# Kernel tuning notes

Measured on AMD Instinct MI355X. Metric: run time of the kernel, lower is better.

Reference implementation:

```python
import jax, jax.numpy as jnp
import numpy as np

LEAK = 0.2   # LeakyReLU slope in CVAE
T = 0.07     # MoCo temperature
TOPK = 2
DISK = 15


def _mlp2(x, Wa, ba, Wb, bb):
    # Linear -> ReLU -> Linear -> ReLU (MoCo encoders)
    return jax.nn.relu(jax.nn.relu(x @ Wa + ba) @ Wb + bb)


def setup_inputs() -> dict:
    key = jax.random.key(0)
    ks = jax.random.split(key, 32)
    B, R, V, F, L = 16384, 512, 1000, 300, 512

    def gn(k, shape, scale=0.05):
        return jax.random.normal(k, shape, dtype=jnp.float32) * scale

    inp = {}
    inp["logits"] = jax.random.normal(ks[0], (B, R), dtype=jnp.float32)
    inp["rels"] = jax.random.randint(ks[1], (R, 2), 0, V, dtype=jnp.int64)
    inp["rel_dict"] = jax.random.normal(ks[2], (V, F), dtype=jnp.float32)
    inp["eps1"] = jax.random.normal(ks[3], (B, L), dtype=jnp.float32)  # eps in ae.forward
    inp["eps2"] = jax.random.normal(ks[4], (B, L), dtype=jnp.float32)  # eps for z_
    # CVAE params (feature_size=300, class_size=300, latent_size=512)
    inp["W1"] = gn(ks[5], (F + F, 512)); inp["b1"] = jnp.zeros((512,), jnp.float32)
    inp["Wmu"] = gn(ks[6], (512, L));   inp["bmu"] = jnp.zeros((L,), jnp.float32)
    inp["Wls"] = gn(ks[7], (512, L));   inp["bls"] = jnp.zeros((L,), jnp.float32)
    inp["W3"] = gn(ks[8], (L + F, 512)); inp["b3"] = jnp.zeros((512,), jnp.float32)
    inp["W4"] = gn(ks[9], (512, F));    inp["b4"] = jnp.zeros((F,), jnp.float32)
    # MoCo encoder_inp (== encoder_k, since momentum update of identical params is a no-op)
    inp["iW1"] = gn(ks[10], (F, 512)); inp["ib1"] = jnp.zeros((512,), jnp.float32)
    inp["iW2"] = gn(ks[11], (512, 512)); inp["ib2"] = jnp.zeros((512,), jnp.float32)
    # MoCo encoder_z
    inp["zW1"] = gn(ks[12], (512, 512)); inp["zb1"] = jnp.zeros((512,), jnp.float32)
    inp["zW2"] = gn(ks[13], (512, 512)); inp["zb2"] = jnp.zeros((512,), jnp.float32)
    return inp


def reference(logits, rels, rel_dict, eps1, eps2,
              W1, b1, Wmu, bmu, Wls, bls, W3, b3, W4, b4,
              iW1, ib1, iW2, ib2, zW1, zb1, zW2, zb2):
    B = logits.shape[0]
    # sort descending / ascending over relation classes
    idx_desc = jnp.argsort(-logits, axis=1)
    idx_asc = jnp.argsort(logits, axis=1)
    top = idx_desc[:, :TOPK]        # [B,2]
    dis = idx_asc[:, :DISK]         # [B,15]

    keys = rels[:, 1]               # [R] indices into rel_dict
    # gathered features are all .detach()-ed in the original code
    pos1 = jax.lax.stop_gradient(rel_dict[keys[top[:, 0]]])   # [B,300]
    pos2 = jax.lax.stop_gradient(rel_dict[keys[top[:, 1]]])   # [B,300]
    neg = jax.lax.stop_gradient(rel_dict[keys[dis]])          # [B,15,300]

    # ---- CVAE forward (batched over B instead of the python loop) ----
    h1 = jax.nn.leaky_relu(jnp.concatenate([pos1, pos2], axis=1) @ W1 + b1, LEAK)
    mu = h1 @ Wmu + bmu              # [B,512]
    log_std = h1 @ Wls + bls         # [B,512]
    std = jnp.exp(log_std)
    z = mu + eps1 * std              # reparametrize inside ae.forward
    h3 = jax.nn.leaky_relu(jnp.concatenate([z, pos2], axis=1) @ W3 + b3, LEAK)
    recon = jnp.tanh(h3 @ W4 + b4)   # [B,300]

    recon_loss = jnp.sum((recon - pos1) ** 2)
    kl_loss = jnp.sum(-0.5 * (1.0 + 2.0 * log_std - mu ** 2 - jnp.exp(2.0 * log_std)))
    loss_vae = (recon_loss + kl_loss).reshape(1)

    z_ = mu + eps2 * std             # second, independent reparametrize for MoCo

    # ---- MoCo forward (batched) ----
    z_p = _mlp2(z_, zW1, zb1, zW2, zb2)                       # [B,512]
    pos_vec = _mlp2(pos1, iW1, ib1, iW2, ib2)                 # [B,512]
    # encoder_k params equal encoder_inp params (copied at init, momentum no-op); no grad
    neg_p = jax.lax.stop_gradient(_mlp2(neg, iW1, ib1, iW2, ib2))  # [B,15,512]

    pos = jnp.sum(z_p * pos_vec, axis=-1, keepdims=True)      # [B,1]
    negl = jnp.einsum('bd,bnd->bn', z_p, neg_p)               # [B,15]
    lg = jnp.concatenate([pos, negl], axis=1) / T             # [B,16]
    # cross entropy with label 0, mean over batch-of-1 then summed over the loop
    loss_csl = jnp.sum(-jax.nn.log_softmax(lg, axis=-1)[:, 0]).reshape(1)

    z_rel = jnp.concatenate([jnp.zeros((1, 512), z_p.dtype), z_p], axis=0)  # [B+1,512]
    return (loss_vae, loss_csl, z_rel)
```

## Files before the change

kernel.cpp:

```cpp
#include <hip/hip_runtime.h>
#include <math.h>

#define B_ 16384
#define R_ 512
#define V_ 1000
#define F_ 300
#define FP_ 320
#define L_ 512
#define H_ 512
#define LEAK_ 0.2f
#define TEMP_ 0.07f
#define DISK_ 15

#define NCSL_BLK (B_ / 4)
#define NKL_BLK  1024
#define NREC_BLK (3 * 128)

typedef short short8 __attribute__((ext_vector_type(8)));
typedef float float4v __attribute__((ext_vector_type(4)));

__device__ __forceinline__ float waveReduceSum(float v) {
#pragma unroll
    for (int off = 32; off; off >>= 1) v += __shfl_xor(v, off);
    return v;
}

__device__ __forceinline__ short f2bf(float f) {
    unsigned u = __float_as_uint(f);
    unsigned r = (u + 0x7FFFu + ((u >> 16) & 1u)) >> 16;
    return (short)r;
}

__device__ __forceinline__ void gld16(const short* g, short* l) {
    __builtin_amdgcn_global_load_lds(
        (const __attribute__((address_space(1))) void*)g,
        (__attribute__((address_space(3))) void*)l, 16, 0, 0);
}

__device__ __forceinline__ void xcd_swizzle(int& bx, int& by) {
    int gx = gridDim.x;
    int nwg = gx * gridDim.y;
    int wg = blockIdx.x + gx * blockIdx.y;
    int cpx = nwg >> 3;
    int swz = (wg & 7) * cpx + (wg >> 3);
    bx = swz % gx;
    by = swz / gx;
}

__device__ __forceinline__ int xcd_swizzle_flat() {
    int nwg = gridDim.x;
    int wg = blockIdx.x;
    int cpx = nwg >> 3;
    return (wg & 7) * cpx + (wg >> 3);
}

__global__ __launch_bounds__(64) void topk_kernel(
    const float* __restrict__ logits, int* __restrict__ top0,
    int* __restrict__ top1, int* __restrict__ dis) {
    int b = blockIdx.x;
    int lane = threadIdx.x;
    const float* lp = logits + (size_t)b * R_;
    float4 va = *(const float4*)&lp[lane * 8];
    float4 vb = *(const float4*)&lp[lane * 8 + 4];
    float v[8] = {va.x, va.y, va.z, va.w, vb.x, vb.y, vb.z, vb.w};
    unsigned u[8];
#pragma unroll
    for (int i = 0; i < 8; ++i) {
        int f = __float_as_int(v[i]);
        u[i] = (unsigned)f ^ ((unsigned)(f >> 31) | 0x80000000u);
    }
    unsigned long long t1 = 0ull, t2 = 0ull;
#pragma unroll
    for (int i = 0; i < 8; ++i) {
        unsigned long long k =
            ((unsigned long long)u[i] << 9) | (unsigned)(511 - (lane * 8 + i));
        if (k > t1) { t2 = t1; t1 = k; }
        else if (k > t2) t2 = k;
    }
#pragma unroll
    for (int off = 32; off; off >>= 1) {
        unsigned long long o1 = __shfl_xor(t1, off);
        unsigned long long o2 = __shfl_xor(t2, off);
        unsigned long long hi = t1 > o1 ? t1 : o1;
        unsigned long long lo = t1 > o1 ? o1 : t1;
        unsigned long long m2 = t2 > o2 ? t2 : o2;
        t1 = hi;
        t2 = lo > m2 ? lo : m2;
    }
    int i0 = 511 - (int)(t1 & 511u);
    int i1 = 511 - (int)(t2 & 511u);

    unsigned k32[8];
#pragma unroll
    for (int i = 0; i < 8; ++i) {
        int idx = lane * 8 + i;
        k32[i] = (u[i] & 0xFFFFFE00u) | (unsigned)idx;
        if (idx == i0 || idx == i1) k32[i] = 0xFFFFFFFFu;
    }
    unsigned lmin = k32[0];
#pragma unroll
    for (int i = 1; i < 8; ++i) lmin = min(lmin, k32[i]);
    int dloc[DISK_];
#pragma unroll
    for (int t = 0; t < DISK_; ++t) {
        unsigned w = lmin;
#pragma unroll
        for (int off = 32; off; off >>= 1) w = min(w, __shfl_xor(w, off));
        int idx = (int)(w & 0x1FFu);
        dloc[t] = idx;
        if ((idx >> 3) == lane) {
            k32[idx & 7] = 0xFFFFFFFFu;
            lmin = k32[0];
#pragma unroll
            for (int i = 1; i < 8; ++i) lmin = min(lmin, k32[i]);
        }
    }
    if (lane == 0) {
        top0[b] = i0; top1[b] = i1;
#pragma unroll
        for (int t = 0; t < DISK_; ++t) dis[b * DISK_ + t] = dloc[t];
    }
}

__global__ __launch_bounds__(FP_) void gather_d(
    const int* __restrict__ rels32, const float* __restrict__ rel_dict,
    float* __restrict__ d_table, short* __restrict__ dt) {
    __shared__ int s_i64;
    int tid = threadIdx.x, r = blockIdx.x;
    if (tid == 0) s_i64 = 1;
    __syncthreads();
    if (rels32[2 * tid + 1] != 0) s_i64 = 0;
    __syncthreads();
    int key = s_i64 ? rels32[4 * r + 2] : rels32[2 * r + 1];
    if (tid < F_) {
        float v = rel_dict[(size_t)key * F_ + tid];
        d_table[(size_t)r * F_ + tid] = v;
        dt[(size_t)r * FP_ + tid] = f2bf(v);
    } else {
        dt[(size_t)r * FP_ + tid] = 0;
    }
}

#define NT_ 11
struct TransArgs {
    const float* W[NT_];
    short* Wt[NT_];
    int row_off[NT_];
    int K[NT_];
    int Kpad[NT_];
    int N[NT_];
    int Npad[NT_];
    int ilv[NT_];
};
__global__ __launch_bounds__(256) void transpose_all(TransArgs ta) {
    int z = blockIdx.z;
    const float* W = ta.W[z];
    short* Wt = ta.Wt[z];
    int row_off = ta.row_off[z];
    int K = ta.K[z], Kpad = ta.Kpad[z], N = ta.N[z], Npad = ta.Npad[z];
    int ilv = ta.ilv[z];
    int k0 = blockIdx.x * 32, n0 = blockIdx.y * 32;
    if (k0 >= Kpad || n0 >= Npad) return;
    __shared__ float tile[32][33];
    int tx = threadIdx.x & 31, ty = threadIdx.x >> 5;
#pragma unroll
    for (int i = 0; i < 4; ++i) {
        int k = k0 + i * 8 + ty, n = n0 + tx;
        tile[i * 8 + ty][tx] = (k < K && n < N) ? W[(size_t)(row_off + k) * N + n] : 0.f;
    }
    __syncthreads();
#pragma unroll
    for (int i = 0; i < 4; ++i) {
        int n = n0 + i * 8 + ty, k = k0 + tx;
        if (n < Npad && k < Kpad) {
            int orow = (ilv >= 0) ? (ilv + 128 * (n >> 6) + (n & 63)) : n;
            Wt[(size_t)orow * Kpad + k] = f2bf(tile[tx][i * 8 + ty]);
        }
    }
}

__global__ __launch_bounds__(256) void h1_kernel(
    const float* __restrict__ Pcat, const float* __restrict__ b1,
    const int* __restrict__ top0, const int* __restrict__ top1,
    short* __restrict__ h1b) {
    int idx = blockIdx.x * 256 + threadIdx.x;
    int b = idx >> 9, j = idx & 511;
    float v = Pcat[(size_t)top0[b] * 2048 + j] + Pcat[(size_t)top1[b] * 2048 + 512 + j] + b1[j];
    h1b[idx] = f2bf(v > 0.f ? v : LEAK_ * v);
}

__global__ __launch_bounds__(256) void ipre_kernel(
    const float* __restrict__ Pcat, const float* __restrict__ ib1,
    short* __restrict__ ipre) {
    int idx = blockIdx.x * 256 + threadIdx.x;
    int r = idx >> 9, j = idx & 511;
    float v = Pcat[(size_t)r * 2048 + 1536 + j] + ib1[j];
    ipre[idx] = f2bf(v > 0.f ? v : 0.f);
}

__device__ __forceinline__ const short8* frag_at(const short* buf, int row, int cb) {
    return (const short8*)&buf[row * 64 + ((cb ^ (row & 7)) * 8)];
}

__device__ __forceinline__ void gemm_core(
    const short* __restrict__ A, const short* __restrict__ Wt,
    int row0, int col0, int tid, short* As0, short* Bs0,
    short* As1, short* Bs1, float4v (&acc)[2][8]) {
    const int K = 512;
    int lane = tid & 63, wv = tid >> 6;
    int lm = lane & 15, q = lane >> 4;
    int rsub = lane >> 3;
    int kswz = ((lane & 7) ^ rsub) * 8;
    int ga = row0 + wv * 8 + rsub;
    int gb = col0 + wv * 8 + rsub;
#pragma unroll
    for (int i = 0; i < 2; ++i)
#pragma unroll
        for (int j = 0; j < 8; ++j) acc[i][j] = {0.f, 0.f, 0.f, 0.f};

    auto STAGE = [&](short* lA, short* lB, int k0) {
#pragma unroll
        for (int j = 0; j < 4; ++j) {
            gld16(&A[(size_t)(ga + 32 * j) * K + k0 + kswz],
                  lA + (wv * 8 + 32 * j) * 64);
            gld16(&Wt[(size_t)(gb + 32 * j) * K + k0 + kswz],
                  lB + (wv * 8 + 32 * j) * 64);
        }
    };

    STAGE(As0, Bs0, 0);
#pragma unroll
    for (int t = 0; t < 8; ++t) {
        short* cA = (t & 1) ? As1 : As0;
        short* cB = (t & 1) ? Bs1 : Bs0;
        short* nA = (t & 1) ? As0 : As1;
        short* nB = (t & 1) ? Bs0 : Bs1;
        if (t < 7) {
            STAGE(nA, nB, (t + 1) * 64);
            asm volatile("s_waitcnt vmcnt(8)" ::: "memory");
        } else {
            asm volatile("s_waitcnt vmcnt(0)" ::: "memory");
        }
        __builtin_amdgcn_s_barrier();
        __builtin_amdgcn_sched_barrier(0);
#pragma unroll
        for (int kk = 0; kk < 2; ++kk) {
            short8 af[2], bf[8];
#pragma unroll
            for (int mt = 0; mt < 2; ++mt)
                af[mt] = *frag_at(cA, wv * 32 + mt * 16 + lm, kk * 4 + q);
#pragma unroll
            for (int nt = 0; nt < 8; ++nt)
                bf[nt] = *frag_at(cB, nt * 16 + lm, kk * 4 + q);
#pragma unroll
            for (int mt = 0; mt < 2; ++mt)
#pragma unroll
                for (int nt = 0; nt < 8; ++nt)
                    acc[mt][nt] = __builtin_amdgcn_mfma_f32_16x16x32_bf16(
                        af[mt], bf[nt], acc[mt][nt], 0, 0, 0);
        }
        __builtin_amdgcn_s_barrier();
    }
}

template <int MODE>
__device__ __forceinline__ void epi_std(
    float4v (&acc)[2][8], int row0, int col0, int tid, void* C,
    const float* __restrict__ bias, const float* __restrict__ table,
    int tld, const int* __restrict__ rowsel) {
    int lane = tid & 63, wv = tid >> 6;
    int lm = lane & 15, q = lane >> 4;
#pragma unroll
    for (int mt = 0; mt < 2; ++mt)
#pragma unroll
        for (int r = 0; r < 4; ++r) {
            int grow = row0 + wv * 32 + mt * 16 + q * 4 + r;
            int trow = (MODE == 1) ? rowsel[grow] : 0;
#pragma unroll
            for (int nt = 0; nt < 8; ++nt) {
                int gcol = col0 + nt * 16 + lm;
                float v = acc[mt][nt][r] + bias[gcol];
                if (MODE == 1) {
                    v += table[(size_t)trow * tld + gcol];
                    v = v > 0.f ? v : LEAK_ * v;
                } else {
                    v = v > 0.f ? v : 0.f;
                }
                if (MODE == 4)
                    ((float*)C)[(size_t)grow * 512 + gcol] = v;
                else
                    ((short*)C)[(size_t)grow * 512 + gcol] = f2bf(v);
            }
        }
}

__device__ __forceinline__ void epi_recon(
    float4v (&acc)[2][8], int row0, int col0, int tid,
    const float* __restrict__ b4, const float* __restrict__ d_table,
    const int* __restrict__ top0, float* __restrict__ p_rec, int pidx,
    float* sred) {
    int lane = tid & 63, wv = tid >> 6;
    int lm = lane & 15, q = lane >> 4;
    float lsum = 0.f;
#pragma unroll
    for (int mt = 0; mt < 2; ++mt)
#pragma unroll
        for (int r = 0; r < 4; ++r) {
            int grow = row0 + wv * 32 + mt * 16 + q * 4 + r;
            int trow = top0[grow];
#pragma unroll
            for (int nt = 0; nt < 8; ++nt) {
                int gcol = col0 + nt * 16 + lm;
                if (gcol < F_) {
                    float v = tanhf(acc[mt][nt][r] + b4[gcol]);
                    float d = v - d_table[(size_t)trow * F_ + gcol];
                    lsum += d * d;
                }
            }
        }
    lsum = waveReduceSum(lsum);
    if (lane == 0) sred[wv] = lsum;
    __syncthreads();
    if (tid == 0) p_rec[pidx] = sred[0] + sred[1] + sred[2] + sred[3];
}

__global__ __launch_bounds__(256) void gemm_muls(
    const short* __restrict__ A, const short* __restrict__ Wt,
    short* __restrict__ Cz, short* __restrict__ Cz2,
    const float* __restrict__ bmu, const float* __restrict__ bls,
    const float* __restrict__ eps1, const float* __restrict__ eps2,
    float* __restrict__ p_kl) {
    __shared__ __align__(16) short As[2][128 * 64];
    __shared__ __align__(16) short Bs[2][128 * 64];
    __shared__ float sred[4];
    int tid = threadIdx.x;
    int bx, by;
    xcd_swizzle(bx, by);
    int row0 = by * 128, col0 = bx * 128;
    float4v acc[2][8];
    gemm_core(A, Wt, row0, col0, tid, As[0], Bs[0], As[1], Bs[1], acc);

    int lane = tid & 63, wv = tid >> 6;
    int lm = lane & 15, q = lane >> 4;
    float kl = 0.f;
#pragma unroll
    for (int mt = 0; mt < 2; ++mt) {
#pragma unroll
        for (int r = 0; r < 4; ++r) {
            int grow = row0 + wv * 32 + mt * 16 + q * 4 + r;
#pragma unroll
            for (int jj = 0; jj < 4; ++jj) {
                int j = (col0 >> 1) + jj * 16 + lm;
                float m = acc[mt][jj][r] + bmu[j];
                float lsv = acc[mt][jj + 4][r] + bls[j];
                float s = __expf(lsv);
                size_t ix = (size_t)grow * 512 + j;
                Cz[ix]  = f2bf(m + eps1[ix] * s);
                Cz2[ix] = f2bf(m + eps2[ix] * s);
                kl += -0.5f * (1.f + 2.f * lsv - m * m - s * s);
            }
        }
    }
    kl = waveReduceSum(kl);
    if (lane == 0) sred[wv] = kl;
    __syncthreads();
    if (tid == 0)
        p_kl[bx + gridDim.x * by] = sred[0] + sred[1] + sred[2] + sred[3];
}

__global__ __launch_bounds__(256) void dual12_kernel(
    const short* __restrict__ zA, const short* __restrict__ Wt3,
    short* __restrict__ h3out, const float* __restrict__ b3,
    const float* __restrict__ Ptab, const int* __restrict__ top1,
    const short* __restrict__ zpA, const short* __restrict__ Wtz1,
    short* __restrict__ tout, const float* __restrict__ zb1,
    const short* __restrict__ ipreA, const short* __restrict__ Wti2,
    float* __restrict__ ipostC, const float* __restrict__ ib2,
    int jobSel) {
    __shared__ __align__(16) short As[2][128 * 64];
    __shared__ __align__(16) short Bs[2][128 * 64];
    int tid = threadIdx.x;
    int wg = xcd_swizzle_flat();
    int job;
    if (jobSel >= 0) {
        job = jobSel;
    } else {
        job = (wg < 512) ? 0 : (wg < 1024 ? 1 : 2);
        wg -= (job == 1) ? 512 : (job == 2 ? 1024 : 0);
    }
    int bx = wg & 3, by = wg >> 2;
    int row0 = by * 128, col0 = bx * 128;
    float4v acc[2][8];
    if (job == 0) {
        gemm_core(zA, Wt3, row0, col0, tid, As[0], Bs[0], As[1], Bs[1], acc);
        epi_std<1>(acc, row0, col0, tid, h3out, b3, Ptab, 2048, top1);
    } else if (job == 1) {
        gemm_core(zpA, Wtz1, row0, col0, tid, As[0], Bs[0], As[1], Bs[1], acc);
        epi_std<2>(acc, row0, col0, tid, tout, zb1, nullptr, 0, nullptr);
    } else {
        gemm_core(ipreA, Wti2, row0, col0, tid, As[0], Bs[0], As[1], Bs[1], acc);
        epi_std<4>(acc, row0, col0, tid, ipostC, ib2, nullptr, 0, nullptr);
    }
}

__global__ __launch_bounds__(256) void dual34_kernel(
    const short* __restrict__ tA, const short* __restrict__ Wtz2,
    float* __restrict__ zpout, const float* __restrict__ zb2,
    const short* __restrict__ h3A, const short* __restrict__ Wt4,
    const float* __restrict__ b4, const float* __restrict__ d_table,
    const int* __restrict__ top0, float* __restrict__ p_rec, int jobSel) {
    __shared__ __align__(16) short As[2][128 * 64];
    __shared__ __align__(16) short Bs[2][128 * 64];
    __shared__ float sred[4];
    int tid = threadIdx.x;
    int wg = xcd_swizzle_flat();
    int job;
    if (jobSel >= 0) {
        job = jobSel;
    } else {
        job = (wg < 512) ? 0 : 1;
        if (job == 1) wg -= 512;
    }
    float4v acc[2][8];
    if (job == 0) {
        int bx = wg & 3, by = wg >> 2;
        int row0 = by * 128, col0 = bx * 128;
        gemm_core(tA, Wtz2, row0, col0, tid, As[0], Bs[0], As[1], Bs[1], acc);
        epi_std<4>(acc, row0, col0, tid, zpout, zb2, nullptr, 0, nullptr);
    } else {
        int bx = wg % 3, by = wg / 3;
        int row0 = by * 128, col0 = bx * 128;
        gemm_core(h3A, Wt4, row0, col0, tid, As[0], Bs[0], As[1], Bs[1], acc);
        epi_recon(acc, row0, col0, tid, b4, d_table, top0, p_rec,
                  bx + 3 * by, sred);
    }
}

template <int EPI, int KK>
__global__ __launch_bounds__(256) void gemm_mfma(
    const short* __restrict__ A, const short* __restrict__ Wt,
    void* __restrict__ C, int ldc, const float* __restrict__ bias,
    const float* __restrict__ table, int tld,
    const int* __restrict__ rowsel, float* __restrict__ lossp, int N) {
    __shared__ __align__(16) short Asl[2][128][40];
    __shared__ __align__(16) short Bsl[2][64][40];
    int tid = threadIdx.x;
    int lane = tid & 63, wv = tid >> 6;
    int lm = lane & 15, q = lane >> 4;
    int bx, by;
    xcd_swizzle(bx, by);
    int row0 = by * 128;
    int col0 = bx * 64;

    float4v acc[2][4];
#pragma unroll
    for (int i = 0; i < 2; ++i)
#pragma unroll
        for (int j = 0; j < 4; ++j) acc[i][j] = {0.f, 0.f, 0.f, 0.f};

    uint4 aReg[2], bReg;
    int ar0 = tid >> 2, ak = (tid & 3) * 8;
    int ar1 = (tid + 256) >> 2;
    int br = tid >> 2, bk = (tid & 3) * 8;

    auto loadG = [&](int k0) {
        aReg[0] = *(const uint4*)&A[(size_t)(row0 + ar0) * KK + k0 + ak];
        aReg[1] = *(const uint4*)&A[(size_t)(row0 + ar1) * KK + k0 + ak];
        bReg    = *(const uint4*)&Wt[(size_t)(col0 + br) * KK + k0 + bk];
    };
    auto storeL = [&](int p) {
        *(uint4*)&Asl[p][ar0][ak] = aReg[0];
        *(uint4*)&Asl[p][ar1][ak] = aReg[1];
        *(uint4*)&Bsl[p][br][bk]  = bReg;
    };

    int p = 0;
    loadG(0);
    storeL(0);
    for (int k0 = 0; k0 < KK; k0 += 32) {
        __syncthreads();
        bool more = (k0 + 32) < KK;
        if (more) loadG(k0 + 32);
        short8 af[2], bfr[4];
#pragma unroll
        for (int mt = 0; mt < 2; ++mt)
            af[mt] = *(const short8*)&Asl[p][wv * 32 + mt * 16 + lm][q * 8];
#pragma unroll
        for (int nt = 0; nt < 4; ++nt)
            bfr[nt] = *(const short8*)&Bsl[p][nt * 16 + lm][q * 8];
#pragma unroll
        for (int mt = 0; mt < 2; ++mt)
#pragma unroll
            for (int nt = 0; nt < 4; ++nt)
                acc[mt][nt] = __builtin_amdgcn_mfma_f32_16x16x32_bf16(
                    af[mt], bfr[nt], acc[mt][nt], 0, 0, 0);
        if (more) { p ^= 1; storeL(p); }
    }

#pragma unroll
    for (int mt = 0; mt < 2; ++mt) {
#pragma unroll
        for (int r = 0; r < 4; ++r) {
            int grow = row0 + wv * 32 + mt * 16 + q * 4 + r;
#pragma unroll
            for (int nt = 0; nt < 4; ++nt) {
                int gcol = col0 + nt * 16 + lm;
                float v = acc[mt][nt][r];
                if (EPI == 4) { v += bias[gcol]; v = v > 0.f ? v : 0.f; }
                ((float*)C)[(size_t)grow * ldc + gcol] = v;
            }
        }
    }
}

__global__ __launch_bounds__(256) void csl_kernel(
    const float* __restrict__ zp, const float* __restrict__ ipost,
    const int* __restrict__ top0, const int* __restrict__ dis,
    float* __restrict__ partial_csl) {
    __shared__ float sred[4];
    int w = threadIdx.x >> 6, lane = threadIdx.x & 63;
    int b = blockIdx.x * 4 + w;
    const float* zr = zp + (size_t)b * 512;
    float z[8];
#pragma unroll
    for (int i = 0; i < 8; ++i) z[i] = zr[i * 64 + lane];
    int cand[16];
    cand[0] = top0[b];
#pragma unroll
    for (int n = 0; n < DISK_; ++n) cand[n + 1] = dis[b * DISK_ + n];
    float s[16];
#pragma unroll
    for (int c = 0; c < 16; ++c) {
        const float* ip = ipost + (size_t)cand[c] * 512;
        float a = 0.f;
#pragma unroll
        for (int i = 0; i < 8; ++i) a += z[i] * ip[i * 64 + lane];
        s[c] = a;
    }
#pragma unroll
    for (int off = 32; off; off >>= 1) {
        float o[16];
#pragma unroll
        for (int c = 0; c < 16; ++c) o[c] = __shfl_xor(s[c], off);
#pragma unroll
        for (int c = 0; c < 16; ++c) s[c] += o[c];
    }
    if (lane == 0) {
        float m = s[0];
#pragma unroll
        for (int c = 1; c < 16; ++c) m = fmaxf(m, s[c]);
        float se = 0.f;
#pragma unroll
        for (int c = 0; c < 16; ++c) se += __expf((s[c] - m) / TEMP_);
        sred[w] = -((s[0] - m) / TEMP_ - __logf(se));
    }
    __syncthreads();
    if (threadIdx.x == 0)
        partial_csl[blockIdx.x] = sred[0] + sred[1] + sred[2] + sred[3];
}

__global__ __launch_bounds__(256) void finalize_kernel(
    const float* __restrict__ pkl, const float* __restrict__ prec,
    const float* __restrict__ pcsl, float* __restrict__ out) {
    __shared__ float red[4][2];
    int tid = threadIdx.x;
    out[2 + tid] = 0.f;
    out[2 + 256 + tid] = 0.f;
    float a0 = 0.f, a1 = 0.f;
    for (int i = tid; i < NKL_BLK; i += 256) a0 += pkl[i];
    for (int i = tid; i < NREC_BLK; i += 256) a0 += prec[i];
    for (int i = tid; i < NCSL_BLK; i += 256) a1 += pcsl[i];
    a0 = waveReduceSum(a0);
    a1 = waveReduceSum(a1);
    int lane = tid & 63, w = tid >> 6;
    if (lane == 0) { red[w][0] = a0; red[w][1] = a1; }
    __syncthreads();
    if (tid == 0) out[0] = red[0][0] + red[1][0] + red[2][0] + red[3][0];
    if (tid == 1) out[1] = red[0][1] + red[1][1] + red[2][1] + red[3][1];
}

extern "C" void kernel_launch(void* const* d_in, const int* in_sizes, int n_in,
                              void* d_out, int out_size, void* d_ws, size_t ws_size,
                              hipStream_t stream) {
    const float* logits  = (const float*)d_in[0];
    const int*   rels    = (const int*)d_in[1];
    const float* rel_dict= (const float*)d_in[2];
    const float* eps1    = (const float*)d_in[3];
    const float* eps2    = (const float*)d_in[4];
    const float* W1  = (const float*)d_in[5];
    const float* b1  = (const float*)d_in[6];
    const float* Wmu = (const float*)d_in[7];
    const float* bmu = (const float*)d_in[8];
    const float* Wls = (const float*)d_in[9];
    const float* bls = (const float*)d_in[10];
    const float* W3  = (const float*)d_in[11];
    const float* b3  = (const float*)d_in[12];
    const float* W4  = (const float*)d_in[13];
    const float* b4  = (const float*)d_in[14];
    const float* iW1 = (const float*)d_in[15];
    const float* ib1 = (const float*)d_in[16];
    const float* iW2 = (const float*)d_in[17];
    const float* ib2 = (const float*)d_in[18];
    const float* zW1 = (const float*)d_in[19];
    const float* zb1 = (const float*)d_in[20];
    const float* zW2 = (const float*)d_in[21];
    const float* zb2 = (const float*)d_in[22];
    float* out = (float*)d_out;

    char* wsp = (char*)d_ws;
    size_t off = 0;
    auto alloc = [&](size_t bytes) { void* p = wsp + off; off += (bytes + 255) & ~(size_t)255; return p; };
    int*   top0    = (int*)alloc(B_ * 4);
    int*   top1    = (int*)alloc(B_ * 4);
    int*   dis     = (int*)alloc(B_ * DISK_ * 4);
    float* d_table = (float*)alloc((size_t)R_ * F_ * 4);
    short* dt      = (short*)alloc((size_t)R_ * FP_ * 2);
    short* Wcat_t  = (short*)alloc((size_t)2048 * FP_ * 2);
    float* Pcat    = (float*)alloc((size_t)R_ * 2048 * 4);
    short* ipre    = (short*)alloc((size_t)R_ * H_ * 2);
    float* ipost   = (float*)alloc((size_t)R_ * H_ * 4);
    short* Wt_muls = (short*)alloc((size_t)1024 * 512 * 2);
    short* Wt_3    = (short*)alloc((size_t)512 * 512 * 2);
    short* Wt_z1   = (short*)alloc((size_t)512 * 512 * 2);
    short* Wt_z2   = (short*)alloc((size_t)512 * 512 * 2);
    short* Wt_4    = (short*)alloc((size_t)384 * 512 * 2);
    short* Wt_i2   = (short*)alloc((size_t)512 * 512 * 2);
    short* bfA     = (short*)alloc((size_t)B_ * H_ * 2);
    short* bfB     = (short*)alloc((size_t)B_ * H_ * 2);
    short* bfC     = (short*)alloc((size_t)B_ * H_ * 2);
    float* p_csl   = (float*)alloc(NCSL_BLK * 4);
    float* p_kl    = (float*)alloc(NKL_BLK * 4);
    float* p_rec   = (float*)alloc(NREC_BLK * 4);
    size_t bfD_bytes = (size_t)B_ * H_ * 2;
    bool merged = (off + bfD_bytes + 256) <= ws_size;
    short* bfD = merged ? (short*)alloc(bfD_bytes) : bfB;

    topk_kernel<<<B_, 64, 0, stream>>>(logits, top0, top1, dis);
    gather_d<<<R_, FP_, 0, stream>>>(rels, rel_dict, d_table, dt);

    TransArgs ta;
    auto set = [&](int i, const float* W, short* Wt, int ro, int K, int Kp, int N, int Np, int ilv) {
        ta.W[i] = W; ta.Wt[i] = Wt; ta.row_off[i] = ro; ta.K[i] = K;
        ta.Kpad[i] = Kp; ta.N[i] = N; ta.Npad[i] = Np; ta.ilv[i] = ilv;
    };
    set(0, Wmu, Wt_muls, 0, 512, 512, 512, 512, 0);
    set(1, Wls, Wt_muls, 0, 512, 512, 512, 512, 64);
    set(2, W3,  Wt_3,  0, 512, 512, 512, 512, -1);
    set(3, zW1, Wt_z1, 0, 512, 512, 512, 512, -1);
    set(4, zW2, Wt_z2, 0, 512, 512, 512, 512, -1);
    set(5, W4,  Wt_4,  0, 512, 512, 300, 384, -1);
    set(6, W1,  Wcat_t,              0,  F_, FP_, 512, 512, -1);
    set(7, W1,  Wcat_t + 512 * FP_,  F_, F_, FP_, 512, 512, -1);
    set(8, W3,  Wcat_t + 1024 * FP_, L_, F_, FP_, 512, 512, -1);
    set(9, iW1, Wcat_t + 1536 * FP_, 0,  F_, FP_, 512, 512, -1);
    set(10, iW2, Wt_i2, 0, 512, 512, 512, 512, -1);
    transpose_all<<<dim3(16, 16, NT_), 256, 0, stream>>>(ta);

    gemm_mfma<5, FP_><<<dim3(32, 4), 256, 0, stream>>>(
        dt, Wcat_t, Pcat, 2048, nullptr, nullptr, 0, nullptr, nullptr, 2048);
    ipre_kernel<<<R_ * H_ / 256, 256, 0, stream>>>(Pcat, ib1, ipre);
    h1_kernel<<<B_ * H_ / 256, 256, 0, stream>>>(Pcat, b1, top0, top1, bfA);

    gemm_muls<<<dim3(8, 128), 256, 0, stream>>>(
        bfA, Wt_muls, bfB, bfC, bmu, bls, eps1, eps2, p_kl);

    if (merged) {
        dual12_kernel<<<1040, 256, 0, stream>>>(
            bfB, Wt_3, bfA, b3, Pcat + 1024, top1,
            bfC, Wt_z1, bfD, zb1,
            ipre, Wt_i2, ipost, ib2, -1);
        dual34_kernel<<<896, 256, 0, stream>>>(
            bfD, Wt_z2, out + 2 + L_, zb2,
            bfA, Wt_4, b4, d_table, top0, p_rec, -1);
    } else {
        dual12_kernel<<<512, 256, 0, stream>>>(
            bfB, Wt_3, bfA, b3, Pcat + 1024, top1,
            bfC, Wt_z1, bfD, zb1, ipre, Wt_i2, ipost, ib2, 0);
        dual12_kernel<<<512, 256, 0, stream>>>(
            bfB, Wt_3, bfA, b3, Pcat + 1024, top1,
            bfC, Wt_z1, bfD, zb1, ipre, Wt_i2, ipost, ib2, 1);
        dual12_kernel<<<16, 256, 0, stream>>>(
            bfB, Wt_3, bfA, b3, Pcat + 1024, top1,
            bfC, Wt_z1, bfD, zb1, ipre, Wt_i2, ipost, ib2, 2);
        dual34_kernel<<<512, 256, 0, stream>>>(
            bfD, Wt_z2, out + 2 + L_, zb2,
            bfA, Wt_4, b4, d_table, top0, p_rec, 0);
        dual34_kernel<<<384, 256, 0, stream>>>(
            bfD, Wt_z2, out + 2 + L_, zb2,
            bfA, Wt_4, b4, d_table, top0, p_rec, 1);
    }

    csl_kernel<<<NCSL_BLK, 256, 0, stream>>>(out + 2 + L_, ipost, top0, dis, p_csl);
    finalize_kernel<<<1, 256, 0, stream>>>(p_kl, p_rec, p_csl, out);
}
```

Baseline: 372.4 us.

## Fuse topk, gather and weight transpose into one front kernel; fold ipre into GEMM epilogue

Merges the top-k/bottom-k selection, relation-embedding gather and batched weight transposition into a single heterogeneous launch of 320-thread blocks dispatched by block index, so the three independent front-end stages run concurrently. The top-k stage now packs five rows per block instead of one. The separate ipre kernel is removed and its bias+ReLU+bf16 conversion is done in the epilogue of the first GEMM through a new EPI mode. This cuts launches and lets small kernels overlap, at the cost of idle threads in the transpose and top-k branches and a larger block size.

```diff
diff --git a/kernel.cpp b/kernel.cpp
--- a/kernel.cpp
+++ b/kernel.cpp
@@ -16,6 +16,11 @@
 #define NKL_BLK  1024
 #define NREC_BLK (3 * 128)
 
+#define NT_ 11
+#define FRONT_TOPK_BLK 3277
+#define FRONT_GATHER_BLK R_
+#define FRONT_TRANS_BLK (16 * 16 * NT_)
+
 typedef short short8 __attribute__((ext_vector_type(8)));
 typedef float float4v __attribute__((ext_vector_type(4)));
 
@@ -54,94 +59,6 @@
     return (wg & 7) * cpx + (wg >> 3);
 }
 
-__global__ __launch_bounds__(64) void topk_kernel(
-    const float* __restrict__ logits, int* __restrict__ top0,
-    int* __restrict__ top1, int* __restrict__ dis) {
-    int b = blockIdx.x;
-    int lane = threadIdx.x;
-    const float* lp = logits + (size_t)b * R_;
-    float4 va = *(const float4*)&lp[lane * 8];
-    float4 vb = *(const float4*)&lp[lane * 8 + 4];
-    float v[8] = {va.x, va.y, va.z, va.w, vb.x, vb.y, vb.z, vb.w};
-    unsigned u[8];
-#pragma unroll
-    for (int i = 0; i < 8; ++i) {
-        int f = __float_as_int(v[i]);
-        u[i] = (unsigned)f ^ ((unsigned)(f >> 31) | 0x80000000u);
-    }
-    unsigned long long t1 = 0ull, t2 = 0ull;
-#pragma unroll
-    for (int i = 0; i < 8; ++i) {
-        unsigned long long k =
-            ((unsigned long long)u[i] << 9) | (unsigned)(511 - (lane * 8 + i));
-        if (k > t1) { t2 = t1; t1 = k; }
-        else if (k > t2) t2 = k;
-    }
-#pragma unroll
-    for (int off = 32; off; off >>= 1) {
-        unsigned long long o1 = __shfl_xor(t1, off);
-        unsigned long long o2 = __shfl_xor(t2, off);
-        unsigned long long hi = t1 > o1 ? t1 : o1;
-        unsigned long long lo = t1 > o1 ? o1 : t1;
-        unsigned long long m2 = t2 > o2 ? t2 : o2;
-        t1 = hi;
-        t2 = lo > m2 ? lo : m2;
-    }
-    int i0 = 511 - (int)(t1 & 511u);
-    int i1 = 511 - (int)(t2 & 511u);
-
-    unsigned k32[8];
-#pragma unroll
-    for (int i = 0; i < 8; ++i) {
-        int idx = lane * 8 + i;
-        k32[i] = (u[i] & 0xFFFFFE00u) | (unsigned)idx;
-        if (idx == i0 || idx == i1) k32[i] = 0xFFFFFFFFu;
-    }
-    unsigned lmin = k32[0];
-#pragma unroll
-    for (int i = 1; i < 8; ++i) lmin = min(lmin, k32[i]);
-    int dloc[DISK_];
-#pragma unroll
-    for (int t = 0; t < DISK_; ++t) {
-        unsigned w = lmin;
-#pragma unroll
-        for (int off = 32; off; off >>= 1) w = min(w, __shfl_xor(w, off));
-        int idx = (int)(w & 0x1FFu);
-        dloc[t] = idx;
-        if ((idx >> 3) == lane) {
-            k32[idx & 7] = 0xFFFFFFFFu;
-            lmin = k32[0];
-#pragma unroll
-            for (int i = 1; i < 8; ++i) lmin = min(lmin, k32[i]);
-        }
-    }
-    if (lane == 0) {
-        top0[b] = i0; top1[b] = i1;
-#pragma unroll
-        for (int t = 0; t < DISK_; ++t) dis[b * DISK_ + t] = dloc[t];
-    }
-}
-
-__global__ __launch_bounds__(FP_) void gather_d(
-    const int* __restrict__ rels32, const float* __restrict__ rel_dict,
-    float* __restrict__ d_table, short* __restrict__ dt) {
-    __shared__ int s_i64;
-    int tid = threadIdx.x, r = blockIdx.x;
-    if (tid == 0) s_i64 = 1;
-    __syncthreads();
-    if (rels32[2 * tid + 1] != 0) s_i64 = 0;
-    __syncthreads();
-    int key = s_i64 ? rels32[4 * r + 2] : rels32[2 * r + 1];
-    if (tid < F_) {
-        float v = rel_dict[(size_t)key * F_ + tid];
-        d_table[(size_t)r * F_ + tid] = v;
-        dt[(size_t)r * FP_ + tid] = f2bf(v);
-    } else {
-        dt[(size_t)r * FP_ + tid] = 0;
-    }
-}
-
-#define NT_ 11
 struct TransArgs {
     const float* W[NT_];
     short* Wt[NT_];
@@ -152,29 +69,136 @@
     int Npad[NT_];
     int ilv[NT_];
 };
-__global__ __launch_bounds__(256) void transpose_all(TransArgs ta) {
-    int z = blockIdx.z;
-    const float* W = ta.W[z];
-    short* Wt = ta.Wt[z];
-    int row_off = ta.row_off[z];
-    int K = ta.K[z], Kpad = ta.Kpad[z], N = ta.N[z], Npad = ta.Npad[z];
-    int ilv = ta.ilv[z];
-    int k0 = blockIdx.x * 32, n0 = blockIdx.y * 32;
-    if (k0 >= Kpad || n0 >= Npad) return;
+
+__device__ void topk_body(int b, int lane, const float* __restrict__ logits,
+                          int* __restrict__ top0, int* __restrict__ top1,
+                          int* __restrict__ dis) {
+    const float* lp = logits + (size_t)b * R_;
+    float4 va = *(const float4*)&lp[lane * 8];
+    float4 vb = *(const float4*)&lp[lane * 8 + 4];
+    float v[8] = {va.x, va.y, va.z, va.w, vb.x, vb.y, vb.z, vb.w};
+    unsigned u[8];
+#pragma unroll
+    for (int i = 0; i < 8; ++i) {
+        int f = __float_as_int(v[i]);
+        u[i] = (unsigned)f ^ ((unsigned)(f >> 31) | 0x80000000u);
+    }
+    unsigned long long t1 = 0ull, t2 = 0ull;
+#pragma unroll
+    for (int i = 0; i < 8; ++i) {
+        unsigned long long k =
+            ((unsigned long long)u[i] << 9) | (unsigned)(511 - (lane * 8 + i));
+        if (k > t1) { t2 = t1; t1 = k; }
+        else if (k > t2) t2 = k;
+    }
+#pragma unroll
+    for (int off = 32; off; off >>= 1) {
+        unsigned long long o1 = __shfl_xor(t1, off);
+        unsigned long long o2 = __shfl_xor(t2, off);
+        unsigned long long hi = t1 > o1 ? t1 : o1;
+        unsigned long long lo = t1 > o1 ? o1 : t1;
+        unsigned long long m2 = t2 > o2 ? t2 : o2;
+        t1 = hi;
+        t2 = lo > m2 ? lo : m2;
+    }
+    int i0 = 511 - (int)(t1 & 511u);
+    int i1 = 511 - (int)(t2 & 511u);
+
+    unsigned k32[8];
+#pragma unroll
+    for (int i = 0; i < 8; ++i) {
+        int idx = lane * 8 + i;
+        k32[i] = (u[i] & 0xFFFFFE00u) | (unsigned)idx;
+        if (idx == i0 || idx == i1) k32[i] = 0xFFFFFFFFu;
+    }
+    unsigned lmin = k32[0];
+#pragma unroll
+    for (int i = 1; i < 8; ++i) lmin = min(lmin, k32[i]);
+    int dloc[DISK_];
+#pragma unroll
+    for (int t = 0; t < DISK_; ++t) {
+        unsigned w = lmin;
+#pragma unroll
+        for (int off = 32; off; off >>= 1) w = min(w, __shfl_xor(w, off));
+        int idx = (int)(w & 0x1FFu);
+        dloc[t] = idx;
+        if ((idx >> 3) == lane) {
+            k32[idx & 7] = 0xFFFFFFFFu;
+            lmin = k32[0];
+#pragma unroll
+            for (int i = 1; i < 8; ++i) lmin = min(lmin, k32[i]);
+        }
+    }
+    if (lane == 0) {
+        top0[b] = i0; top1[b] = i1;
+#pragma unroll
+        for (int t = 0; t < DISK_; ++t) dis[b * DISK_ + t] = dloc[t];
+    }
+}
+
+__global__ __launch_bounds__(320) void front_kernel(
+    const float* __restrict__ logits, int* __restrict__ top0,
+    int* __restrict__ top1, int* __restrict__ dis,
+    const int* __restrict__ rels32, const float* __restrict__ rel_dict,
+    float* __restrict__ d_table, short* __restrict__ dt, TransArgs ta) {
     __shared__ float tile[32][33];
-    int tx = threadIdx.x & 31, ty = threadIdx.x >> 5;
-#pragma unroll
-    for (int i = 0; i < 4; ++i) {
-        int k = k0 + i * 8 + ty, n = n0 + tx;
-        tile[i * 8 + ty][tx] = (k < K && n < N) ? W[(size_t)(row_off + k) * N + n] : 0.f;
-    }
-    __syncthreads();
-#pragma unroll
-    for (int i = 0; i < 4; ++i) {
-        int n = n0 + i * 8 + ty, k = k0 + tx;
-        if (n < Npad && k < Kpad) {
-            int orow = (ilv >= 0) ? (ilv + 128 * (n >> 6) + (n & 63)) : n;
-            Wt[(size_t)orow * Kpad + k] = f2bf(tile[tx][i * 8 + ty]);
+    __shared__ int s_i64;
+    int blk = blockIdx.x;
+    int tid = threadIdx.x;
+
+    if (blk < FRONT_TOPK_BLK) {
+        int b = blk * 5 + (tid >> 6);
+        if (b < B_) topk_body(b, tid & 63, logits, top0, top1, dis);
+        return;
+    }
+    blk -= FRONT_TOPK_BLK;
+    if (blk < FRONT_GATHER_BLK) {
+        int r = blk;
+        if (tid == 0) s_i64 = 1;
+        __syncthreads();
+        if (rels32[2 * tid + 1] != 0) s_i64 = 0;
+        __syncthreads();
+        int key = s_i64 ? rels32[4 * r + 2] : rels32[2 * r + 1];
+        if (tid < F_) {
+            float v = rel_dict[(size_t)key * F_ + tid];
+            d_table[(size_t)r * F_ + tid] = v;
+            dt[(size_t)r * FP_ + tid] = f2bf(v);
+        } else {
+            dt[(size_t)r * FP_ + tid] = 0;
+        }
+        return;
+    }
+    blk -= FRONT_GATHER_BLK;
+    {
+        int z = blk >> 8;
+        int kx = blk & 15, ny = (blk >> 4) & 15;
+        const float* W = ta.W[z];
+        short* Wt = ta.Wt[z];
+        int row_off = ta.row_off[z];
+        int K = ta.K[z], Kpad = ta.Kpad[z], N = ta.N[z], Npad = ta.Npad[z];
+        int ilv = ta.ilv[z];
+        int k0 = kx * 32, n0 = ny * 32;
+        bool live = (k0 < Kpad) && (n0 < Npad);
+        bool act = live && (tid < 256);
+        int tx = tid & 31, ty = tid >> 5;
+        if (act) {
+#pragma unroll
+            for (int i = 0; i < 4; ++i) {
+                int k = k0 + i * 8 + ty, n = n0 + tx;
+                tile[i * 8 + ty][tx] =
+                    (k < K && n < N) ? W[(size_t)(row_off + k) * N + n] : 0.f;
+            }
+        }
+        __syncthreads();
+        if (act) {
+#pragma unroll
+            for (int i = 0; i < 4; ++i) {
+                int n = n0 + i * 8 + ty, k = k0 + tx;
+                if (n < Npad && k < Kpad) {
+                    int orow = (ilv >= 0) ? (ilv + 128 * (n >> 6) + (n & 63)) : n;
+                    Wt[(size_t)orow * Kpad + k] = f2bf(tile[tx][i * 8 + ty]);
+                }
+            }
         }
     }
 }
@@ -187,15 +211,6 @@
     int b = idx >> 9, j = idx & 511;
     float v = Pcat[(size_t)top0[b] * 2048 + j] + Pcat[(size_t)top1[b] * 2048 + 512 + j] + b1[j];
     h1b[idx] = f2bf(v > 0.f ? v : LEAK_ * v);
-}
-
-__global__ __launch_bounds__(256) void ipre_kernel(
-    const float* __restrict__ Pcat, const float* __restrict__ ib1,
-    short* __restrict__ ipre) {
-    int idx = blockIdx.x * 256 + threadIdx.x;
-    int r = idx >> 9, j = idx & 511;
-    float v = Pcat[(size_t)r * 2048 + 1536 + j] + ib1[j];
-    ipre[idx] = f2bf(v > 0.f ? v : 0.f);
 }
 
 __device__ __forceinline__ const short8* frag_at(const short* buf, int row, int cb) {
@@ -497,6 +512,7 @@
         if (more) { p ^= 1; storeL(p); }
     }
 
+    short* ipre_out = (EPI == 6) ? (short*)lossp : nullptr;
 #pragma unroll
     for (int mt = 0; mt < 2; ++mt) {
 #pragma unroll
@@ -508,6 +524,11 @@
                 float v = acc[mt][nt][r];
                 if (EPI == 4) { v += bias[gcol]; v = v > 0.f ? v : 0.f; }
                 ((float*)C)[(size_t)grow * ldc + gcol] = v;
+                if (EPI == 6 && gcol >= 1536) {
+                    int j = gcol - 1536;
+                    float w = v + bias[j];
+                    ipre_out[(size_t)grow * 512 + j] = f2bf(w > 0.f ? w : 0.f);
+                }
             }
         }
     }
@@ -635,9 +656,6 @@
     bool merged = (off + bfD_bytes + 256) <= ws_size;
     short* bfD = merged ? (short*)alloc(bfD_bytes) : bfB;
 
-    topk_kernel<<<B_, 64, 0, stream>>>(logits, top0, top1, dis);
-    gather_d<<<R_, FP_, 0, stream>>>(rels, rel_dict, d_table, dt);
-
     TransArgs ta;
     auto set = [&](int i, const float* W, short* Wt, int ro, int K, int Kp, int N, int Np, int ilv) {
         ta.W[i] = W; ta.Wt[i] = Wt; ta.row_off[i] = ro; ta.K[i] = K;
@@ -654,11 +672,13 @@
     set(8, W3,  Wcat_t + 1024 * FP_, L_, F_, FP_, 512, 512, -1);
     set(9, iW1, Wcat_t + 1536 * FP_, 0,  F_, FP_, 512, 512, -1);
     set(10, iW2, Wt_i2, 0, 512, 512, 512, 512, -1);
-    transpose_all<<<dim3(16, 16, NT_), 256, 0, stream>>>(ta);
-
-    gemm_mfma<5, FP_><<<dim3(32, 4), 256, 0, stream>>>(
-        dt, Wcat_t, Pcat, 2048, nullptr, nullptr, 0, nullptr, nullptr, 2048);
-    ipre_kernel<<<R_ * H_ / 256, 256, 0, stream>>>(Pcat, ib1, ipre);
+
+    front_kernel<<<FRONT_TOPK_BLK + FRONT_GATHER_BLK + FRONT_TRANS_BLK,
+                   320, 0, stream>>>(
+        logits, top0, top1, dis, rels, rel_dict, d_table, dt, ta);
+
+    gemm_mfma<6, FP_><<<dim3(32, 4), 256, 0, stream>>>(
+        dt, Wcat_t, Pcat, 2048, ib1, nullptr, 0, nullptr, (float*)ipre, 2048);
     h1_kernel<<<B_ * H_ / 256, 256, 0, stream>>>(Pcat, b1, top0, top1, bfA);
 
     gemm_muls<<<dim3(8, 128), 256, 0, stream>>>(
```

Result: slower. 392.0 us, median of 2 (+5.3%).
